# Optimization experiments

Measured on AMD Instinct MI355X. Metric: run time of the kernel, lower is better.

## Reference

```python
import jax, jax.numpy as jnp
import numpy as np

EPS = 1e-13

def setup_inputs() -> dict:
    key = jax.random.key(0)
    k1, k2, k3 = jax.random.split(key, 3)
    B, L, H = 64, 512, 1024
    sentence = jax.random.normal(k1, (B, L, H), dtype=jnp.float32)
    mask = jax.random.uniform(k2, (B, L), dtype=jnp.float32)
    attention_matrix = jax.random.normal(k3, (B, L, L), dtype=jnp.float32)
    return {"sentence": sentence, "mask": mask, "attention_matrix": attention_matrix}

def reference(sentence, mask, attention_matrix):
    # stable softmax over last dim of [B, L, L]
    attention_weights = jax.nn.softmax(attention_matrix, axis=-1)
    # mask rows: mask is [B, L] -> [B, L, 1]
    attention_weights = attention_weights * mask[:, :, None]
    # renormalize over last dim
    attention_weights = attention_weights / (attention_weights.sum(-1, keepdims=True) + EPS)
    # weighted sum: [B, L, L] @ [B, L, H] -> [B, L, H]
    return jnp.einsum('bij,bjh->bih', attention_weights, sentence)
```

## Files before the change

kernel.cpp:

```cpp
#include <hip/hip_runtime.h>
#include <hip/hip_bf16.h>

#define B_ 64
#define L_ 512
#define H_ 1024
#define EPS_ 1e-13f

typedef unsigned short u16;
typedef __attribute__((ext_vector_type(8))) short s16x8;
typedef __attribute__((ext_vector_type(4))) float f32x4;

__device__ __forceinline__ u16 f2bf(float f) {
  __hip_bfloat16 h = __float2bfloat16(f);
  union { __hip_bfloat16 h; u16 u; } c; c.h = h; return c.u;
}

__global__ __launch_bounds__(256) void softmax_rows(const float* __restrict__ att,
                                                    const float* __restrict__ mask,
                                                    u16* __restrict__ Wout) {
  const int w = threadIdx.x >> 6, lane = threadIdx.x & 63;
  const int row0 = blockIdx.x * 16 + w * 4;

  float a[4][8];
#pragma unroll
  for (int r = 0; r < 4; ++r) {
    const float* p = att + (size_t)(row0 + r) * L_ + lane * 8;
    float4 v0 = *(const float4*)p;
    float4 v1 = *(const float4*)(p + 4);
    a[r][0] = v0.x; a[r][1] = v0.y; a[r][2] = v0.z; a[r][3] = v0.w;
    a[r][4] = v1.x; a[r][5] = v1.y; a[r][6] = v1.z; a[r][7] = v1.w;
  }

  float m[4];
#pragma unroll
  for (int r = 0; r < 4; ++r) {
    m[r] = a[r][0];
#pragma unroll
    for (int j = 1; j < 8; ++j) m[r] = fmaxf(m[r], a[r][j]);
  }
#pragma unroll
  for (int off = 32; off > 0; off >>= 1)
#pragma unroll
    for (int r = 0; r < 4; ++r) m[r] = fmaxf(m[r], __shfl_xor(m[r], off));

  float z[4] = {0.f, 0.f, 0.f, 0.f};
#pragma unroll
  for (int r = 0; r < 4; ++r)
#pragma unroll
    for (int j = 0; j < 8; ++j) { a[r][j] = __expf(a[r][j] - m[r]); z[r] += a[r][j]; }
#pragma unroll
  for (int off = 32; off > 0; off >>= 1)
#pragma unroll
    for (int r = 0; r < 4; ++r) z[r] += __shfl_xor(z[r], off);

#pragma unroll
  for (int r = 0; r < 4; ++r) {
    const float mk = mask[row0 + r];
    const float c = (1.0f / z[r]) * (mk / (mk + EPS_));
    union { u16 u[8]; uint4 v; } wv;
#pragma unroll
    for (int j = 0; j < 8; ++j) wv.u[j] = f2bf(a[r][j] * c);
    *(uint4*)(Wout + (size_t)(row0 + r) * L_ + lane * 8) = wv.v;
  }
}

#define GLOAD(gp, lp)                                                              \
  __builtin_amdgcn_global_load_lds((const __attribute__((address_space(1))) unsigned*)(gp), \
                                   (__attribute__((address_space(3))) unsigned*)(void*)(lp), 16, 0, 0)

__global__ __launch_bounds__(512, 2) void gemm_xd(const u16* __restrict__ Wm,
                                                  const float* __restrict__ X,
                                                  float* __restrict__ out) {
  const int NT = 16;
  const int swz = (blockIdx.x & 7) * 64 + (blockIdx.x >> 3);
  const int b  = swz >> 3;
  const int mt = (swz >> 2) & 1;
  const int nt = swz & 3;

  __shared__ __align__(16) char lds[147456];

  const int t = threadIdx.x;
  const int lane = t & 63;
  const int w = t >> 6;
  const int wm = w >> 2, wn = w & 3;

  const u16* gW = Wm + ((size_t)b * L_ + mt * 256) * L_;
  const float* gX = X + (size_t)b * L_ * H_ + nt * 256;

  const int r0 = t >> 2;
  const int xsw = (r0 & 3) ^ ((r0 >> 2) & 3);
  const int scol = ((t & 3) ^ xsw) * 8;
  const u16* pA0 = gW + (size_t)r0 * L_ + scol;
  char* dA = lds + w * 1024;

  const float* pXw = gX + (size_t)w * H_;
  const int l4  = lane * 4;
  const int lx4 = (lane ^ 4) * 4;
  char* dBw = lds + 49152 + w * 1024;

  int offA[8];
#pragma unroll
  for (int mf = 0; mf < 8; ++mf) {
    int r = wm * 128 + mf * 16 + (lane & 15);
    offA[mf] = r * 64 + ((((lane >> 4) ^ (r & 3) ^ ((r >> 2) & 3))) << 4);
  }
  int offBc[4];
#pragma unroll
  for (int nf = 0; nf < 4; ++nf) {
    int n = wn * 64 + nf * 16 + (lane & 15);
    int oct = lane >> 4;
    offBc[nf] = oct * 8192 + ((n ^ ((oct & 1) << 4)) << 2);
  }

  f32x4 acc[8][4] = {};

#define A_ISSUE(tt)                                                        \
  do {                                                                     \
    GLOAD(pA0 + (tt) * 32, dA + ((tt) % 3) * 16384);                       \
    GLOAD(pA0 + (tt) * 32 + 128 * (size_t)L_, dA + ((tt) % 3) * 16384 + 8192); \
  } while (0)

#define B_ISSUE(tt)                                                        \
  do {                                                                     \
    GLOAD(pXw + (size_t)((tt) * 32 + 0)  * H_ + l4,  dBw + ((tt) % 3) * 32768);         \
    GLOAD(pXw + (size_t)((tt) * 32 + 8)  * H_ + lx4, dBw + ((tt) % 3) * 32768 + 8192);  \
    GLOAD(pXw + (size_t)((tt) * 32 + 16) * H_ + l4,  dBw + ((tt) % 3) * 32768 + 16384); \
    GLOAD(pXw + (size_t)((tt) * 32 + 24) * H_ + lx4, dBw + ((tt) % 3) * 32768 + 24576); \
  } while (0)

  A_ISSUE(0); B_ISSUE(0); A_ISSUE(1); B_ISSUE(1);
  asm volatile("s_waitcnt vmcnt(6)" ::: "memory");
  __builtin_amdgcn_s_barrier();

#pragma unroll
  for (int k = 0; k < NT; ++k) {
    if (k + 2 < NT) { A_ISSUE(k + 2); B_ISSUE(k + 2); }

    const char* baseA = lds + (k % 3) * 16384;
    const char* baseB = lds + 49152 + (k % 3) * 32768;

    s16x8 af[8];
#pragma unroll
    for (int mf = 0; mf < 8; ++mf) af[mf] = *(const s16x8*)(baseA + offA[mf]);

    s16x8 bf4[4];
#pragma unroll
    for (int nf = 0; nf < 4; ++nf) {
      union { u16 u[8]; s16x8 v; } pk;
#pragma unroll
      for (int j = 0; j < 8; ++j)
        pk.u[j] = f2bf(*(const float*)(baseB + offBc[nf] + j * 1024));
      bf4[nf] = pk.v;
    }
    asm volatile("s_waitcnt lgkmcnt(0)" ::: "memory");

    __builtin_amdgcn_s_setprio(1);
#pragma unroll
    for (int mf = 0; mf < 8; ++mf)
#pragma unroll
      for (int nf = 0; nf < 4; ++nf)
        acc[mf][nf] = __builtin_amdgcn_mfma_f32_16x16x32_bf16(af[mf], bf4[nf], acc[mf][nf], 0, 0, 0);
    __builtin_amdgcn_s_setprio(0);

    if (k + 1 < NT) {
      if (k + 2 < NT) asm volatile("s_waitcnt vmcnt(6)" ::: "memory");
      else            asm volatile("s_waitcnt vmcnt(0)" ::: "memory");
      __builtin_amdgcn_s_barrier();
    }
  }
#undef A_ISSUE
#undef B_ISSUE

  const int orow0 = mt * 256 + wm * 128 + ((lane >> 4) << 2);
  const int ocol0 = nt * 256 + wn * 64 + (lane & 15);
#pragma unroll
  for (int mf = 0; mf < 8; ++mf)
#pragma unroll
    for (int nf = 0; nf < 4; ++nf)
#pragma unroll
      for (int j = 0; j < 4; ++j) {
        int row = orow0 + mf * 16 + j;
        int col = ocol0 + nf * 16;
        out[((size_t)b * L_ + row) * H_ + col] = acc[mf][nf][j];
      }
}

extern "C" void kernel_launch(void* const* d_in, const int* in_sizes, int n_in,
                              void* d_out, int out_size, void* d_ws, size_t ws_size,
                              hipStream_t stream) {
  (void)in_sizes; (void)n_in; (void)out_size; (void)ws_size;
  const float* sent = (const float*)d_in[0];
  const float* mask = (const float*)d_in[1];
  const float* att  = (const float*)d_in[2];
  u16* Wm = (u16*)d_ws;
  float* outp = (float*)d_out;

  softmax_rows<<<2048, 256, 0, stream>>>(att, mask, Wm);
  gemm_xd<<<B_ * 2 * 4, 512, 0, stream>>>(Wm, sent, outp);
}
```

Baseline: 93.75 us.

## Shrink GEMM tile to 256x128 with double buffering for higher occupancy

```diff
diff --git a/kernel.cpp b/kernel.cpp
--- a/kernel.cpp
+++ b/kernel.cpp
@@ -68,80 +68,79 @@
   __builtin_amdgcn_global_load_lds((const __attribute__((address_space(1))) unsigned*)(gp), \
                                    (__attribute__((address_space(3))) unsigned*)(void*)(lp), 16, 0, 0)
 
-__global__ __launch_bounds__(512, 2) void gemm_xd(const u16* __restrict__ Wm,
+__global__ __launch_bounds__(512, 4) void gemm_xd(const u16* __restrict__ Wm,
                                                   const float* __restrict__ X,
                                                   float* __restrict__ out) {
   const int NT = 16;
-  const int swz = (blockIdx.x & 7) * 64 + (blockIdx.x >> 3);
-  const int b  = swz >> 3;
-  const int mt = (swz >> 2) & 1;
-  const int nt = swz & 3;
+  const int lg = (blockIdx.x & 7) * 128 + (blockIdx.x >> 3);
+  const int mt = lg & 1;
+  const int nt = (lg >> 1) & 7;
+  const int b  = lg >> 4;
 
-  __shared__ __align__(16) char lds[147456];
+  __shared__ __align__(16) char lds[65536];
 
   const int t = threadIdx.x;
   const int lane = t & 63;
   const int w = t >> 6;
-  const int wm = w >> 2, wn = w & 3;
+  const int wm = w >> 1, wn = w & 1;
 
   const u16* gW = Wm + ((size_t)b * L_ + mt * 256) * L_;
-  const float* gX = X + (size_t)b * L_ * H_ + nt * 256;
+  const float* gX = X + (size_t)b * L_ * H_ + nt * 128;
 
-  const int r0 = t >> 2;
-  const int xsw = (r0 & 3) ^ ((r0 >> 2) & 3);
-  const int scol = ((t & 3) ^ xsw) * 8;
-  const u16* pA0 = gW + (size_t)r0 * L_ + scol;
+  const int ar = t >> 2;
+  const int ascol = ((t & 3) ^ ((ar & 3) ^ ((ar >> 2) & 3))) * 8;
+  const u16* pA0 = gW + (size_t)ar * L_ + ascol;
   char* dA = lds + w * 1024;
 
-  const float* pXw = gX + (size_t)w * H_;
-  const int l4  = lane * 4;
-  const int lx4 = (lane ^ 4) * 4;
-  char* dBw = lds + 49152 + w * 1024;
+  const int bodd = (w >= 4) ? 4 : 0;
+  const int bq = ((lane & 31) ^ bodd) * 4;
+  const int brow = w * 2 + (lane >> 5);
+  char* dB = lds + 32768 + w * 1024;
 
-  int offA[8];
+  int offA[4];
 #pragma unroll
-  for (int mf = 0; mf < 8; ++mf) {
-    int r = wm * 128 + mf * 16 + (lane & 15);
+  for (int mf = 0; mf < 4; ++mf) {
+    int r = wm * 64 + mf * 16 + (lane & 15);
     offA[mf] = r * 64 + ((((lane >> 4) ^ (r & 3) ^ ((r >> 2) & 3))) << 4);
   }
-  int offBc[4];
+  int offB[4];
 #pragma unroll
   for (int nf = 0; nf < 4; ++nf) {
     int n = wn * 64 + nf * 16 + (lane & 15);
     int oct = lane >> 4;
-    offBc[nf] = oct * 8192 + ((n ^ ((oct & 1) << 4)) << 2);
+    offB[nf] = 32768 + oct * 4096 + ((n ^ ((oct & 1) << 4)) << 2);
   }
 
-  f32x4 acc[8][4] = {};
+  f32x4 acc[4][4] = {};
 
-#define A_ISSUE(tt)                                                        \
-  do {                                                                     \
-    GLOAD(pA0 + (tt) * 32, dA + ((tt) % 3) * 16384);                       \
-    GLOAD(pA0 + (tt) * 32 + 128 * (size_t)L_, dA + ((tt) % 3) * 16384 + 8192); \
+#define A_ISSUE(tt)                                                         \
+  do {                                                                      \
+    GLOAD(pA0 + (tt) * 32, dA + ((tt) & 1) * 16384);                        \
+    GLOAD(pA0 + (tt) * 32 + 128 * (size_t)L_, dA + ((tt) & 1) * 16384 + 8192); \
   } while (0)
 
-#define B_ISSUE(tt)                                                        \
-  do {                                                                     \
-    GLOAD(pXw + (size_t)((tt) * 32 + 0)  * H_ + l4,  dBw + ((tt) % 3) * 32768);         \
-    GLOAD(pXw + (size_t)((tt) * 32 + 8)  * H_ + lx4, dBw + ((tt) % 3) * 32768 + 8192);  \
-    GLOAD(pXw + (size_t)((tt) * 32 + 16) * H_ + l4,  dBw + ((tt) % 3) * 32768 + 16384); \
-    GLOAD(pXw + (size_t)((tt) * 32 + 24) * H_ + lx4, dBw + ((tt) % 3) * 32768 + 24576); \
+#define B_ISSUE(tt)                                                         \
+  do {                                                                      \
+    GLOAD(gX + (size_t)((tt) * 32 + brow) * H_ + bq,                        \
+          dB + ((tt) & 1) * 16384);                                         \
+    GLOAD(gX + (size_t)((tt) * 32 + 16 + brow) * H_ + bq,                   \
+          dB + ((tt) & 1) * 16384 + 8192);                                  \
   } while (0)
 
-  A_ISSUE(0); B_ISSUE(0); A_ISSUE(1); B_ISSUE(1);
-  asm volatile("s_waitcnt vmcnt(6)" ::: "memory");
+  A_ISSUE(0); B_ISSUE(0);
+  asm volatile("s_waitcnt vmcnt(0)" ::: "memory");
   __builtin_amdgcn_s_barrier();
 
 #pragma unroll
   for (int k = 0; k < NT; ++k) {
-    if (k + 2 < NT) { A_ISSUE(k + 2); B_ISSUE(k + 2); }
+    if (k + 1 < NT) { A_ISSUE(k + 1); B_ISSUE(k + 1); }
 
-    const char* baseA = lds + (k % 3) * 16384;
-    const char* baseB = lds + 49152 + (k % 3) * 32768;
+    const char* baseA = lds + (k & 1) * 16384;
+    const char* baseB = lds + (k & 1) * 16384;
 
-    s16x8 af[8];
+    s16x8 af[4];
 #pragma unroll
-    for (int mf = 0; mf < 8; ++mf) af[mf] = *(const s16x8*)(baseA + offA[mf]);
+    for (int mf = 0; mf < 4; ++mf) af[mf] = *(const s16x8*)(baseA + offA[mf]);
 
     s16x8 bf4[4];
 #pragma unroll
@@ -149,32 +148,31 @@
       union { u16 u[8]; s16x8 v; } pk;
 #pragma unroll
       for (int j = 0; j < 8; ++j)
-        pk.u[j] = f2bf(*(const float*)(baseB + offBc[nf] + j * 1024));
+        pk.u[j] = f2bf(*(const float*)(baseB + offB[nf] + j * 512));
       bf4[nf] = pk.v;
     }
     asm volatile("s_waitcnt lgkmcnt(0)" ::: "memory");
 
     __builtin_amdgcn_s_setprio(1);
 #pragma unroll
-    for (int mf = 0; mf < 8; ++mf)
+    for (int mf = 0; mf < 4; ++mf)
 #pragma unroll
       for (int nf = 0; nf < 4; ++nf)
         acc[mf][nf] = __builtin_amdgcn_mfma_f32_16x16x32_bf16(af[mf], bf4[nf], acc[mf][nf], 0, 0, 0);
     __builtin_amdgcn_s_setprio(0);
 
     if (k + 1 < NT) {
-      if (k + 2 < NT) asm volatile("s_waitcnt vmcnt(6)" ::: "memory");
-      else            asm volatile("s_waitcnt vmcnt(0)" ::: "memory");
+      asm volatile("s_waitcnt vmcnt(0)" ::: "memory");
       __builtin_amdgcn_s_barrier();
     }
   }
 #undef A_ISSUE
 #undef B_ISSUE
 
-  const int orow0 = mt * 256 + wm * 128 + ((lane >> 4) << 2);
-  const int ocol0 = nt * 256 + wn * 64 + (lane & 15);
+  const int orow0 = mt * 256 + wm * 64 + ((lane >> 4) << 2);
+  const int ocol0 = nt * 128 + wn * 64 + (lane & 15);
 #pragma unroll
-  for (int mf = 0; mf < 8; ++mf)
+  for (int mf = 0; mf < 4; ++mf)
 #pragma unroll
     for (int nf = 0; nf < 4; ++nf)
 #pragma unroll
@@ -196,5 +194,5 @@
   float* outp = (float*)d_out;
 
   softmax_rows<<<2048, 256, 0, stream>>>(att, mask, Wm);
-  gemm_xd<<<B_ * 2 * 4, 512, 0, stream>>>(Wm, sent, outp);
+  gemm_xd<<<B_ * 2 * 8, 512, 0, stream>>>(Wm, sent, outp);
 }
```

Result: slower. 109.2 us (+16.5%).
